# Performance work log

Hardware: AMD Instinct MI355X
Metric: run time of the kernel (lower is better)

## Reference

```python
import jax, jax.numpy as jnp
import numpy as np

NUM_CAMS = 1
NUM_HEADS = 1
NUM_LEVELS = 1
NUM_POINTS = 4
NUM_DEPTH = 128
EMBED = 128  # must equal NUM_DEPTH (output_proj is applied to the depth axis)


def setup_inputs() -> dict:
    key0 = jax.random.key(0)
    ks = jax.random.split(key0, 12)
    bsv, nq, nv = 1, 1024, 1024  # nq == nv == H*W (32*32)
    off_dim = NUM_CAMS * NUM_HEADS * NUM_LEVELS * NUM_DEPTH * NUM_POINTS * 2  # 1024
    aw_dim = NUM_CAMS * NUM_HEADS * NUM_LEVELS * NUM_DEPTH * NUM_POINTS       # 512
    return {
        "query": jax.random.normal(ks[0], (bsv, nq, EMBED), jnp.float32),
        "key": jax.random.normal(ks[1], (NUM_CAMS, nv, bsv, EMBED), jnp.float32),
        "value": jax.random.normal(ks[2], (NUM_CAMS, nv, bsv, EMBED), jnp.float32),
        "ref_3d": jax.random.uniform(ks[3], (bsv * NUM_CAMS, nq * NUM_DEPTH, 2), jnp.float32),
        "spatial_shapes": jnp.array([[32, 32]], dtype=jnp.int32),
        "W_off": jax.random.normal(ks[4], (EMBED, off_dim), jnp.float32) * 0.02,
        "b_off": jax.random.normal(ks[5], (off_dim,), jnp.float32) * 0.02,
        "W_attn": jax.random.normal(ks[6], (EMBED, aw_dim), jnp.float32) * 0.02,
        "b_attn": jax.random.normal(ks[7], (aw_dim,), jnp.float32) * 0.02,
        "W_v": jax.random.normal(ks[8], (EMBED, EMBED), jnp.float32) / np.sqrt(EMBED),
        "b_v": jnp.zeros((EMBED,), jnp.float32),
        "W_o": jax.random.normal(ks[9], (EMBED, EMBED), jnp.float32) / np.sqrt(EMBED),
        "b_o": jnp.zeros((EMBED,), jnp.float32),
    }


def _bilinear_sample(val, H, W, x, y):
    """grid_sample(align_corners=False, padding=zeros) equivalent.
    val: [B, H*W, D]; x, y: [B, Q, P] in pixel coords. Returns [B, Q, P, D]."""
    B, Q, P = x.shape
    D = val.shape[-1]
    x0f = jnp.floor(x); y0f = jnp.floor(y)
    ix0 = x0f.astype(jnp.int32); iy0 = y0f.astype(jnp.int32)
    wx1 = x - x0f; wy1 = y - y0f
    wx0 = 1.0 - wx1; wy0 = 1.0 - wy1

    def corner(ix, iy, w):
        valid = (ix >= 0) & (ix < W) & (iy >= 0) & (iy < H)
        idx = jnp.clip(iy, 0, H - 1) * W + jnp.clip(ix, 0, W - 1)  # [B,Q,P]
        g = jnp.take_along_axis(val, idx.reshape(B, Q * P)[:, :, None], axis=1)
        g = g.reshape(B, Q, P, D)
        return g * (w * valid.astype(val.dtype))[..., None]

    return (corner(ix0, iy0, wx0 * wy0)
            + corner(ix0 + 1, iy0, wx1 * wy0)
            + corner(ix0, iy0 + 1, wx0 * wy1)
            + corner(ix0 + 1, iy0 + 1, wx1 * wy1))


def reference(query, key, value, ref_3d, spatial_shapes,
              W_off, b_off, W_attn, b_attn, W_v, b_v, W_o, b_o):
    bsv, nq, E = query.shape
    cams, nv, bs, _ = key.shape
    identity = query

    # key/value: [cams, nv, bs, E] -> [bsv, nv, E]
    key2 = jnp.transpose(key, (2, 0, 1, 3)).reshape(bsv, nv, E)
    val = jnp.flip(value, axis=0)
    val = jnp.transpose(val, (2, 0, 1, 3)).reshape(bsv, nv, E)
    val = val @ W_v + b_v
    val = val.reshape(bsv * cams, nv, E)  # num_heads=1 -> head_dim=E

    # offsets / attention weights (heads=levels=1 axes squeezed)
    off = (query @ W_off + b_off).reshape(bsv, nq, cams, NUM_DEPTH, NUM_POINTS, 2)
    aw = (query @ W_attn + b_attn).reshape(bsv, nq, cams, NUM_DEPTH, NUM_LEVELS * NUM_POINTS)
    aw = jax.nn.softmax(aw, axis=-1).reshape(bsv, nq, cams, NUM_DEPTH, NUM_POINTS)
    off = jnp.transpose(off, (0, 2, 1, 3, 4, 5)).reshape(bsv * cams, nq * NUM_DEPTH, NUM_POINTS, 2)
    aw = jnp.transpose(aw, (0, 2, 1, 3, 4)).reshape(bsv * cams, nq * NUM_DEPTH, NUM_POINTS)

    H = spatial_shapes[0, 0]
    W = spatial_shapes[0, 1]
    norm = jnp.stack([W, H]).astype(off.dtype)  # [W, H]
    loc = ref_3d[:, :, None, :] + off / norm    # [B, Qe, P, 2] in [0,1]
    x = loc[..., 0] * W.astype(loc.dtype) - 0.5
    y = loc[..., 1] * H.astype(loc.dtype) - 0.5

    sampled = _bilinear_sample(val, H, W, x, y)          # [B, Qe, P, E]
    out = jnp.einsum('bqpe,bqp->bqe', sampled, aw)       # weighted sum over points

    out = out.reshape(bsv, cams, nq, NUM_DEPTH, E).mean(axis=1)  # [bsv, nq, depth, E]
    out = (out * key2[:, :, None, :]).mean(axis=-1)              # [bsv, nq, depth]
    out = out @ W_o + b_o                                        # depth == EMBED
    return out + identity  # dropout = identity in eval
```

## Files before the change

### kernel.cpp

```cpp
#include <hip/hip_runtime.h>


#define NQ   1024
#define NV   1024
#define ND   128
#define NP   4
#define IMG_W 32
#define IMG_H 32
#define QB   4

typedef __attribute__((ext_vector_type(8))) short bfx8;
typedef __attribute__((ext_vector_type(4))) float f32x4;

__device__ __forceinline__ unsigned short bf_rne(float f) {
  unsigned u = __float_as_uint(f);
  return (unsigned short)((u + 0x7FFFu + ((u >> 16) & 1u)) >> 16);
}
__device__ __forceinline__ float bf2f(unsigned short u) {
  return __uint_as_float((unsigned)u << 16);
}

__device__ __forceinline__ bfx8 pack8(const float* p) {
  bfx8 v;
#pragma unroll
  for (int j = 0; j < 8; ++j) v[j] = (short)bf_rne(p[j]);
  return v;
}

__global__ __launch_bounds__(512) void mono_kernel(
    const float* __restrict__ query, const float* __restrict__ key,
    const float* __restrict__ value, const float* __restrict__ ref3d,
    const float* __restrict__ W_off, const float* __restrict__ b_off,
    const float* __restrict__ W_attn, const float* __restrict__ b_attn,
    const float* __restrict__ W_v, const float* __restrict__ b_v,
    const float* __restrict__ W_o, const float* __restrict__ b_o,
    float* __restrict__ out) {
  __shared__ float q_lds[QB][128];
  __shared__ float key_lds[QB][128];
  __shared__ float keyp_lds[QB][128];
  __shared__ float c_lds[QB];
  __shared__ unsigned short img_bf[QB][NV];
  __shared__ unsigned short off_bf[QB][1024];
  __shared__ unsigned short aw_bf[QB][512];
  __shared__ __align__(16) unsigned short sval[128 * 128];
  float* o1s = (float*)sval;

  const int tid = threadIdx.x;
  const int q0 = blockIdx.x * QB;
  const int w = tid >> 6, l = tid & 63;

  if (tid < 128) {
    ((float4*)q_lds)[tid] = ((const float4*)(query + (size_t)q0 * 128))[tid];
  } else if (tid < 256) {
    ((float4*)key_lds)[tid - 128] =
        ((const float4*)(key + (size_t)q0 * 128))[tid - 128];
  }
  __syncthreads();

  {
    float2 aoff[QB];
    float aaw[QB];
#pragma unroll
    for (int qq = 0; qq < QB; ++qq) {
      aoff[qq] = make_float2(0.f, 0.f);
      aaw[qq] = 0.f;
    }
    const float* wo_p = W_off + (size_t)tid * 2;
    const float* wa_p = W_attn + tid;
#pragma unroll 4
    for (int e4 = 0; e4 < 32; ++e4) {
      float4 q4[QB];
#pragma unroll
      for (int qq = 0; qq < QB; ++qq)
        q4[qq] = *(const float4*)(&q_lds[qq][e4 * 4]);
#pragma unroll
      for (int j = 0; j < 4; ++j) {
        const int e = e4 * 4 + j;
        const float2 w2 = *(const float2*)(wo_p + (size_t)e * 1024);
        const float wa = wa_p[(size_t)e * 512];
#pragma unroll
        for (int qq = 0; qq < QB; ++qq) {
          const float* qp = (const float*)&q4[qq];
          const float qv = qp[j];
          aoff[qq].x = fmaf(qv, w2.x, aoff[qq].x);
          aoff[qq].y = fmaf(qv, w2.y, aoff[qq].y);
          aaw[qq] = fmaf(qv, wa, aaw[qq]);
        }
      }
    }
    const float2 bo2 = *(const float2*)(b_off + tid * 2);
    const float ba = b_attn[tid];
#pragma unroll
    for (int qq = 0; qq < QB; ++qq) {
      const unsigned px = (unsigned)bf_rne(aoff[qq].x + bo2.x) |
                          ((unsigned)bf_rne(aoff[qq].y + bo2.y) << 16);
      *(unsigned*)(&off_bf[qq][tid * 2]) = px;
      aw_bf[qq][tid] = bf_rne(aaw[qq] + ba);
    }
  }

  {
#pragma unroll
    for (int it = 0; it < 4; ++it) {
      const int c = tid + it * 512;
      const int r = c >> 4, cc = c & 15;
      const bfx8 v = pack8(W_v + (size_t)r * 128 + cc * 8);
      const int byte = r * 256 + ((cc * 16) ^ ((r & 15) << 4));
      *(bfx8*)((char*)sval + byte) = v;
    }
    bfx8 afK[4];
    {
      const int row = l & 15, g = l >> 4;
#pragma unroll
      for (int ks = 0; ks < 4; ++ks) {
        bfx8 a;
        if (row < QB) {
          a = pack8(&key_lds[row][ks * 32 + g * 8]);
        } else {
#pragma unroll
          for (int j = 0; j < 8; ++j) a[j] = 0;
        }
        afK[ks] = a;
      }
    }
    __syncthreads();

    {
      const int col = l & 15, g = l >> 4;
      const int r = w * 16 + col;
      f32x4 acc = {0.f, 0.f, 0.f, 0.f};
#pragma unroll
      for (int ks = 0; ks < 4; ++ks) {
        const int colb = (ks * 64 + g * 16) ^ (col << 4);
        const bfx8 bfr = *(const bfx8*)((const char*)sval + r * 256 + colb);
        acc = __builtin_amdgcn_mfma_f32_16x16x32_bf16(afK[ks], bfr, acc,
                                                      0, 0, 0);
      }
      if (g == 0) {
#pragma unroll
        for (int i = 0; i < QB; ++i) keyp_lds[i][r] = acc[i];
      }
    }
    if (tid < QB) {
      float s = 0.f;
      for (int e = 0; e < 128; e += 4) {
        const float4 bv = *(const float4*)(b_v + e);
        const float4 k4 = *(const float4*)(&key_lds[tid][e]);
        s = fmaf(bv.x, k4.x,
            fmaf(bv.y, k4.y, fmaf(bv.z, k4.z, fmaf(bv.w, k4.w, s))));
      }
      c_lds[tid] = s;
    }
  }
  __syncthreads();

  bfx8 afrag[4];
  {
    const int row = l & 15, g = l >> 4;
#pragma unroll
    for (int ks = 0; ks < 4; ++ks) {
      bfx8 a;
      if (row < QB) {
        a = pack8(&keyp_lds[row][ks * 32 + g * 8]);
      } else {
#pragma unroll
        for (int j = 0; j < 8; ++j) a[j] = 0;
      }
      afrag[ks] = a;
    }
  }
  __syncthreads();

  for (int vt = 0; vt < 8; ++vt) {
#pragma unroll
    for (int it = 0; it < 4; ++it) {
      const int c = tid + it * 512;
      const int r = c >> 4, cc = c & 15;
      const bfx8 v = pack8(value + (size_t)(vt * 128 + r) * 128 + cc * 8);
      const int byte = r * 256 + ((cc * 16) ^ ((r & 15) << 4));
      *(bfx8*)((char*)sval + byte) = v;
    }
    __syncthreads();

    {
      const int col = l & 15, g = l >> 4;
      const int r = w * 16 + col;
      f32x4 acc = {0.f, 0.f, 0.f, 0.f};
#pragma unroll
      for (int ks = 0; ks < 4; ++ks) {
        const int colb = (ks * 64 + g * 16) ^ (col << 4);
        const bfx8 bfr = *(const bfx8*)((const char*)sval + r * 256 + colb);
        acc = __builtin_amdgcn_mfma_f32_16x16x32_bf16(afrag[ks], bfr, acc,
                                                      0, 0, 0);
      }
      if (g == 0) {
        const int v = vt * 128 + r;
#pragma unroll
        for (int i = 0; i < QB; ++i)
          img_bf[i][v] = bf_rne(acc[i] + c_lds[i]);
      }
    }
    __syncthreads();
  }

  {
    const int qq = tid >> 7;
    const int q = q0 + qq;
    const int d = tid & 127;
    const unsigned short* im = img_bf[qq];
    const size_t qe = (size_t)q * ND + d;

    const float rx = ref3d[qe * 2 + 0];
    const float ry = ref3d[qe * 2 + 1];

    const uint2 ua = *(const uint2*)(&aw_bf[qq][d * 4]);
    const float a0 = bf2f((unsigned short)(ua.x & 0xffff));
    const float a1 = bf2f((unsigned short)(ua.x >> 16));
    const float a2 = bf2f((unsigned short)(ua.y & 0xffff));
    const float a3 = bf2f((unsigned short)(ua.y >> 16));
    const float mx = fmaxf(fmaxf(a0, a1), fmaxf(a2, a3));
    const float e0 = __expf(a0 - mx), e1 = __expf(a1 - mx),
                e2 = __expf(a2 - mx), e3 = __expf(a3 - mx);
    const float inv = 1.0f / (e0 + e1 + e2 + e3);
    const float wgt4[4] = {e0 * inv, e1 * inv, e2 * inv, e3 * inv};

    const uint4 uo = *(const uint4*)(&off_bf[qq][d * 8]);
    const unsigned ox[4] = {uo.x, uo.y, uo.z, uo.w};

    float acc = 0.0f;
#pragma unroll
    for (int p = 0; p < NP; ++p) {
      const float x = rx * (float)IMG_W + bf2f((unsigned short)(ox[p] & 0xffff)) - 0.5f;
      const float y = ry * (float)IMG_H + bf2f((unsigned short)(ox[p] >> 16)) - 0.5f;
      const float xf = floorf(x), yf = floorf(y);
      const int ix0 = (int)xf, iy0 = (int)yf;
      const float wx1 = x - xf, wy1 = y - yf;
      const float wx0 = 1.0f - wx1, wy0 = 1.0f - wy1;

      float s = 0.0f;
#pragma unroll
      for (int cy = 0; cy < 2; ++cy) {
#pragma unroll
        for (int cx = 0; cx < 2; ++cx) {
          const int ix = ix0 + cx, iy = iy0 + cy;
          const bool valid = (ix >= 0) & (ix < IMG_W) & (iy >= 0) & (iy < IMG_H);
          const int cix = min(max(ix, 0), IMG_W - 1);
          const int ciy = min(max(iy, 0), IMG_H - 1);
          const float wgt = (cx ? wx1 : wx0) * (cy ? wy1 : wy0);
          s += valid ? bf2f(im[ciy * IMG_W + cix]) * wgt : 0.0f;
        }
      }
      acc += wgt4[p] * s;
    }
    __syncthreads();
    o1s[qq * ND + d] = acc * (1.0f / 128.0f);
  }
  __syncthreads();

  {
    const int qq = tid >> 7;
    const int n = tid & 127;
    float acc = b_o[n] + q_lds[qq][n];
#pragma unroll 8
    for (int d = 0; d < 128; ++d)
      acc = fmaf(o1s[qq * ND + d], W_o[(size_t)d * 128 + n], acc);
    out[(size_t)(q0 + qq) * 128 + n] = acc;
  }
}

extern "C" void kernel_launch(void* const* d_in, const int* in_sizes, int n_in,
                              void* d_out, int out_size, void* d_ws, size_t ws_size,
                              hipStream_t stream) {
  const float* query  = (const float*)d_in[0];
  const float* key    = (const float*)d_in[1];
  const float* value  = (const float*)d_in[2];
  const float* ref3d  = (const float*)d_in[3];
  const float* W_off  = (const float*)d_in[5];
  const float* b_off  = (const float*)d_in[6];
  const float* W_attn = (const float*)d_in[7];
  const float* b_attn = (const float*)d_in[8];
  const float* W_v    = (const float*)d_in[9];
  const float* b_v    = (const float*)d_in[10];
  const float* W_o    = (const float*)d_in[11];
  const float* b_o    = (const float*)d_in[12];
  float* out = (float*)d_out;

  mono_kernel<<<NQ / QB, 512, 0, stream>>>(query, key, value, ref3d,
                                           W_off, b_off, W_attn, b_attn,
                                           W_v, b_v, W_o, b_o, out);
}
```

Measured before the change: 108.2 us.

## Warp-specialize offset/attn projection and value projection to run concurrently

Splits the block's warps so four warps compute the offset and attention-weight projections (now four outputs per thread with wider loads) while the other four stream value tiles into private LDS buffers and run the MFMA value projection without block-wide barriers. W_v staging moves before the first barrier, and an unnecessary barrier before the o1s write is removed. This targets the serialized phases and the per-tile __syncthreads in the value loop, at the cost of halving the threads available to each phase.

```diff
diff --git a/kernel.cpp b/kernel.cpp
--- a/kernel.cpp
+++ b/kernel.cpp
@@ -19,7 +19,6 @@
 __device__ __forceinline__ float bf2f(unsigned short u) {
   return __uint_as_float((unsigned)u << 16);
 }
-
 __device__ __forceinline__ bfx8 pack8(const float* p) {
   bfx8 v;
 #pragma unroll
@@ -48,6 +47,7 @@
   const int tid = threadIdx.x;
   const int q0 = blockIdx.x * QB;
   const int w = tid >> 6, l = tid & 63;
+  const int col = l & 15, g = l >> 4;
 
   if (tid < 128) {
     ((float4*)q_lds)[tid] = ((const float4*)(query + (size_t)q0 * 128))[tid];
@@ -55,78 +55,30 @@
     ((float4*)key_lds)[tid - 128] =
         ((const float4*)(key + (size_t)q0 * 128))[tid - 128];
   }
+#pragma unroll
+  for (int it = 0; it < 4; ++it) {
+    const int c = tid + it * 512;
+    const int r = c >> 4, cc = c & 15;
+    const bfx8 v = pack8(W_v + (size_t)r * 128 + cc * 8);
+    const int byte = r * 256 + ((cc * 16) ^ ((r & 15) << 4));
+    *(bfx8*)((char*)sval + byte) = v;
+  }
   __syncthreads();
 
   {
-    float2 aoff[QB];
-    float aaw[QB];
-#pragma unroll
-    for (int qq = 0; qq < QB; ++qq) {
-      aoff[qq] = make_float2(0.f, 0.f);
-      aaw[qq] = 0.f;
-    }
-    const float* wo_p = W_off + (size_t)tid * 2;
-    const float* wa_p = W_attn + tid;
-#pragma unroll 4
-    for (int e4 = 0; e4 < 32; ++e4) {
-      float4 q4[QB];
-#pragma unroll
-      for (int qq = 0; qq < QB; ++qq)
-        q4[qq] = *(const float4*)(&q_lds[qq][e4 * 4]);
-#pragma unroll
-      for (int j = 0; j < 4; ++j) {
-        const int e = e4 * 4 + j;
-        const float2 w2 = *(const float2*)(wo_p + (size_t)e * 1024);
-        const float wa = wa_p[(size_t)e * 512];
-#pragma unroll
-        for (int qq = 0; qq < QB; ++qq) {
-          const float* qp = (const float*)&q4[qq];
-          const float qv = qp[j];
-          aoff[qq].x = fmaf(qv, w2.x, aoff[qq].x);
-          aoff[qq].y = fmaf(qv, w2.y, aoff[qq].y);
-          aaw[qq] = fmaf(qv, wa, aaw[qq]);
-        }
-      }
-    }
-    const float2 bo2 = *(const float2*)(b_off + tid * 2);
-    const float ba = b_attn[tid];
-#pragma unroll
-    for (int qq = 0; qq < QB; ++qq) {
-      const unsigned px = (unsigned)bf_rne(aoff[qq].x + bo2.x) |
-                          ((unsigned)bf_rne(aoff[qq].y + bo2.y) << 16);
-      *(unsigned*)(&off_bf[qq][tid * 2]) = px;
-      aw_bf[qq][tid] = bf_rne(aaw[qq] + ba);
-    }
-  }
-
-  {
-#pragma unroll
-    for (int it = 0; it < 4; ++it) {
-      const int c = tid + it * 512;
-      const int r = c >> 4, cc = c & 15;
-      const bfx8 v = pack8(W_v + (size_t)r * 128 + cc * 8);
-      const int byte = r * 256 + ((cc * 16) ^ ((r & 15) << 4));
-      *(bfx8*)((char*)sval + byte) = v;
-    }
     bfx8 afK[4];
+#pragma unroll
+    for (int ks = 0; ks < 4; ++ks) {
+      bfx8 a;
+      if (col < QB) {
+        a = pack8(&key_lds[col][ks * 32 + g * 8]);
+      } else {
+#pragma unroll
+        for (int j = 0; j < 8; ++j) a[j] = 0;
+      }
+      afK[ks] = a;
+    }
     {
-      const int row = l & 15, g = l >> 4;
-#pragma unroll
-      for (int ks = 0; ks < 4; ++ks) {
-        bfx8 a;
-        if (row < QB) {
-          a = pack8(&key_lds[row][ks * 32 + g * 8]);
-        } else {
-#pragma unroll
-          for (int j = 0; j < 8; ++j) a[j] = 0;
-        }
-        afK[ks] = a;
-      }
-    }
-    __syncthreads();
-
-    {
-      const int col = l & 15, g = l >> 4;
       const int r = w * 16 + col;
       f32x4 acc = {0.f, 0.f, 0.f, 0.f};
 #pragma unroll
@@ -154,54 +106,104 @@
   }
   __syncthreads();
 
-  bfx8 afrag[4];
-  {
-    const int row = l & 15, g = l >> 4;
+  if (w < 4) {
+    const int t = tid;
+    float4 aoff[QB];
+    float2 aaw[QB];
+#pragma unroll
+    for (int qq = 0; qq < QB; ++qq) {
+      aoff[qq] = make_float4(0.f, 0.f, 0.f, 0.f);
+      aaw[qq] = make_float2(0.f, 0.f);
+    }
+    const float* wo_p = W_off + (size_t)t * 4;
+    const float* wa_p = W_attn + (size_t)t * 2;
+#pragma unroll 4
+    for (int e4 = 0; e4 < 32; ++e4) {
+      float4 q4[QB];
+#pragma unroll
+      for (int qq = 0; qq < QB; ++qq)
+        q4[qq] = *(const float4*)(&q_lds[qq][e4 * 4]);
+#pragma unroll
+      for (int j = 0; j < 4; ++j) {
+        const int e = e4 * 4 + j;
+        const float4 w4 = *(const float4*)(wo_p + (size_t)e * 1024);
+        const float2 w2 = *(const float2*)(wa_p + (size_t)e * 512);
+#pragma unroll
+        for (int qq = 0; qq < QB; ++qq) {
+          const float* qp = (const float*)&q4[qq];
+          const float qv = qp[j];
+          aoff[qq].x = fmaf(qv, w4.x, aoff[qq].x);
+          aoff[qq].y = fmaf(qv, w4.y, aoff[qq].y);
+          aoff[qq].z = fmaf(qv, w4.z, aoff[qq].z);
+          aoff[qq].w = fmaf(qv, w4.w, aoff[qq].w);
+          aaw[qq].x = fmaf(qv, w2.x, aaw[qq].x);
+          aaw[qq].y = fmaf(qv, w2.y, aaw[qq].y);
+        }
+      }
+    }
+    const float4 bo4 = *(const float4*)(b_off + t * 4);
+    const float2 ba2 = *(const float2*)(b_attn + t * 2);
+#pragma unroll
+    for (int qq = 0; qq < QB; ++qq) {
+      const unsigned lo = (unsigned)bf_rne(aoff[qq].x + bo4.x) |
+                          ((unsigned)bf_rne(aoff[qq].y + bo4.y) << 16);
+      const unsigned hi = (unsigned)bf_rne(aoff[qq].z + bo4.z) |
+                          ((unsigned)bf_rne(aoff[qq].w + bo4.w) << 16);
+      *(uint2*)(&off_bf[qq][t * 4]) = make_uint2(lo, hi);
+      *(unsigned*)(&aw_bf[qq][t * 2]) =
+          (unsigned)bf_rne(aaw[qq].x + ba2.x) |
+          ((unsigned)bf_rne(aaw[qq].y + ba2.y) << 16);
+    }
+  } else {
+    const int ww = w - 4;
+    unsigned short* buf = sval + ww * 4096;
+    bfx8 afrag[4];
 #pragma unroll
     for (int ks = 0; ks < 4; ++ks) {
       bfx8 a;
-      if (row < QB) {
-        a = pack8(&keyp_lds[row][ks * 32 + g * 8]);
+      if (col < QB) {
+        a = pack8(&keyp_lds[col][ks * 32 + g * 8]);
       } else {
 #pragma unroll
         for (int j = 0; j < 8; ++j) a[j] = 0;
       }
       afrag[ks] = a;
     }
-  }
-  __syncthreads();
-
-  for (int vt = 0; vt < 8; ++vt) {
-#pragma unroll
-    for (int it = 0; it < 4; ++it) {
-      const int c = tid + it * 512;
-      const int r = c >> 4, cc = c & 15;
-      const bfx8 v = pack8(value + (size_t)(vt * 128 + r) * 128 + cc * 8);
-      const int byte = r * 256 + ((cc * 16) ^ ((r & 15) << 4));
-      *(bfx8*)((char*)sval + byte) = v;
-    }
-    __syncthreads();
-
-    {
-      const int col = l & 15, g = l >> 4;
-      const int r = w * 16 + col;
-      f32x4 acc = {0.f, 0.f, 0.f, 0.f};
-#pragma unroll
-      for (int ks = 0; ks < 4; ++ks) {
-        const int colb = (ks * 64 + g * 16) ^ (col << 4);
-        const bfx8 bfr = *(const bfx8*)((const char*)sval + r * 256 + colb);
-        acc = __builtin_amdgcn_mfma_f32_16x16x32_bf16(afrag[ks], bfr, acc,
-                                                      0, 0, 0);
-      }
-      if (g == 0) {
-        const int v = vt * 128 + r;
-#pragma unroll
-        for (int i = 0; i < QB; ++i)
-          img_bf[i][v] = bf_rne(acc[i] + c_lds[i]);
-      }
-    }
-    __syncthreads();
-  }
+    float cq[QB];
+#pragma unroll
+    for (int i = 0; i < QB; ++i) cq[i] = c_lds[i];
+
+    for (int sub = 0; sub < 8; ++sub) {
+      const int vbase = ww * 256 + sub * 32;
+#pragma unroll
+      for (int it = 0; it < 8; ++it) {
+        const int c = l + it * 64;
+        const int r = c >> 4, cc = c & 15;
+        const bfx8 v = pack8(value + (size_t)(vbase + r) * 128 + cc * 8);
+        const int byte = r * 256 + ((cc * 16) ^ ((r & 15) << 4));
+        *(bfx8*)((char*)buf + byte) = v;
+      }
+#pragma unroll
+      for (int cg = 0; cg < 2; ++cg) {
+        const int r = cg * 16 + col;
+        f32x4 acc = {0.f, 0.f, 0.f, 0.f};
+#pragma unroll
+        for (int ks = 0; ks < 4; ++ks) {
+          const int colb = (ks * 64 + g * 16) ^ (col << 4);
+          const bfx8 bfr = *(const bfx8*)((const char*)buf + r * 256 + colb);
+          acc = __builtin_amdgcn_mfma_f32_16x16x32_bf16(afrag[ks], bfr, acc,
+                                                        0, 0, 0);
+        }
+        if (g == 0) {
+          const int v = vbase + r;
+#pragma unroll
+          for (int i = 0; i < QB; ++i)
+            img_bf[i][v] = bf_rne(acc[i] + cq[i]);
+        }
+      }
+    }
+  }
+  __syncthreads();
 
   {
     const int qq = tid >> 7;
@@ -252,8 +254,7 @@
       }
       acc += wgt4[p] * s;
     }
-    __syncthreads();
-    o1s[qq * ND + d] = acc * (1.0f / 128.0f);
+    o1s[qq * ND + (tid & 127)] = acc * (1.0f / 128.0f);
   }
   __syncthreads();
 
```

New measurement: 102.0 us. 1.06x faster.
